# Performance work log

Hardware: AMD Instinct MI355X
Metric: run time of the kernel (lower is better)

The kernel has to match this reference:

```python
import jax, jax.numpy as jnp
import numpy as np

B, T, V, E, H, C = 128, 256, 50000, 300, 512, 11
START, STOP = 9, 10
NEG = -100000.0


def _lstm_dir(x, mask, w_ih, w_hh, b_ih, b_hh, reverse):
    # x: [B,T,D]; precompute input-to-gate projection for all timesteps
    gx = jnp.einsum('btd,gd->btg', x, w_ih) + b_ih + b_hh
    m = mask
    if reverse:
        gx = gx[:, ::-1]
        m = m[:, ::-1]
    Bc = x.shape[0]
    Hh = w_hh.shape[1]

    def step(carry, inp):
        h, c = carry
        g, mt = inp
        gates = g + h @ w_hh.T  # [B,4H]
        i, f, gg, o = jnp.split(gates, 4, axis=-1)
        i = jax.nn.sigmoid(i)
        f = jax.nn.sigmoid(f)
        o = jax.nn.sigmoid(o)
        gg = jnp.tanh(gg)
        c_new = f * c + i * gg
        h_new = o * jnp.tanh(c_new)
        mt = mt[:, None]
        h = jnp.where(mt, h_new, h)  # packed-sequence semantics: hold state on pads
        c = jnp.where(mt, c_new, c)
        return (h, c), h

    init = (jnp.zeros((Bc, Hh), x.dtype), jnp.zeros((Bc, Hh), x.dtype))
    _, hs = jax.lax.scan(step, init, (gx.transpose(1, 0, 2), m.T))
    hs = hs.transpose(1, 0, 2)
    if reverse:
        hs = hs[:, ::-1]
    # pad_packed_sequence zeroes padded positions
    return hs * mask[..., None].astype(x.dtype)


def _encode(tokens, mask, embeddings, params):
    x = embeddings[tokens]
    for (wif, whf, bif, bhf, wir, whr, bir, bhr) in params:
        fwd = _lstm_dir(x, mask, wif, whf, bif, bhf, False)
        bwd = _lstm_dir(x, mask, wir, whr, bir, bhr, True)
        x = jnp.concatenate([fwd, bwd], -1)
    return x


def _viterbi(emis, mask, transitions, seq_len):
    def vstep(scores, inp):
        emi, mt = inp
        cand = scores[:, :, None] + transitions[None]  # [B,C,C]
        bt = jnp.argmax(cand, axis=1)
        new = jnp.max(cand, axis=1) + emi
        return jnp.where(mt[:, None], new, scores), bt

    scores0 = jnp.zeros_like(emis[:, 0, :])
    final, backtrack = jax.lax.scan(vstep, scores0, (emis.transpose(1, 0, 2), mask.T))
    final = final + transitions[:, STOP][None]
    best_last = jnp.argmax(final, axis=-1)  # [B]

    ls = jnp.arange(emis.shape[1] - 1, -1, -1)

    def btstep(cur, inp):
        bt_l, l = inp
        emit = jnp.where(l < seq_len, cur, 0)  # pad tail with 0 as in original
        prev = jnp.take_along_axis(bt_l, cur[:, None], axis=1)[:, 0]
        cur = jnp.where((l >= 1) & (l <= seq_len - 1), prev, cur)
        return cur, emit

    _, emits = jax.lax.scan(btstep, best_last, (backtrack[::-1], ls))
    return emits[::-1].T  # [B,T]


def _nll(emis, tags, mask, transitions, seq_len):
    # CRF forward algorithm (replicates original init with -1e5 full scores)
    def fstep(scores, inp):
        emi, mt = inp
        new = jax.nn.logsumexp(scores[:, :, None] + emi[:, None, :] + transitions[None], axis=1)
        return jnp.where(mt[:, None], new, scores), None

    scores0 = jnp.full_like(emis[:, 0, :], NEG)
    final, _ = jax.lax.scan(fstep, scores0, (emis.transpose(1, 0, 2), mask.T))
    fwd_score = jax.nn.logsumexp(final + transitions[:, STOP][None], axis=-1, keepdims=True)

    em_sc = jnp.take_along_axis(emis, tags[..., None], -1)[..., 0]  # [B,T]
    y_aug = jnp.concatenate([jnp.full((tags.shape[0], 1), START, tags.dtype), tags], 1)
    tr_sc = transitions[y_aug[:, :-1], y_aug[:, 1:]]  # [B,T]
    last_tag = jnp.take_along_axis(y_aug, seq_len[:, None], 1)
    last_tr = transitions[last_tag[:, 0], STOP][:, None]
    mf = mask.astype(emis.dtype)
    gold = (mf * (em_sc + tr_sc)).sum(-1, keepdims=True) + last_tr
    return (fwd_score - gold).mean()


def setup_inputs() -> dict:
    key = jax.random.key(0)
    ks = iter(jax.random.split(key, 40))
    sl = jax.random.randint(next(ks), (B,), 1, T + 1)
    sl = -jnp.sort(-sl.at[0].set(T))  # descending, max == T (pack_padded requirement)
    mask = jnp.arange(T)[None, :] < sl[:, None]
    tokens = jax.random.randint(next(ks), (B, T), 0, V)
    tags = jax.random.randint(next(ks), (B, T), 0, 9)
    s = 1.0 / float(np.sqrt(H))

    def u(shape):
        return jax.random.uniform(next(ks), shape, jnp.float32, -s, s)

    inp = dict(tokens=tokens, seq_len=sl, mask=mask, tags=tags,
               embeddings=jax.random.normal(next(ks), (V, E), jnp.float32) * 0.1)
    G = 4 * H
    for li, d in enumerate([E, 2 * H]):
        for suf in ['', 'r']:
            inp[f'w_ih_l{li}{suf}'] = u((G, d))
            inp[f'w_hh_l{li}{suf}'] = u((G, H))
            inp[f'b_ih_l{li}{suf}'] = u((G,))
            inp[f'b_hh_l{li}{suf}'] = u((G,))
    inp['fc_w'] = u((C, 2 * H))
    inp['fc_b'] = u((C,))
    tr = jax.random.normal(next(ks), (C, C), jnp.float32)
    inp['transitions'] = tr.at[START, :].set(-1.0).at[:, STOP].set(-1.0)
    return inp


def reference(tokens, seq_len, mask, tags, embeddings,
              w_ih_l0, w_hh_l0, b_ih_l0, b_hh_l0,
              w_ih_l0r, w_hh_l0r, b_ih_l0r, b_hh_l0r,
              w_ih_l1, w_hh_l1, b_ih_l1, b_hh_l1,
              w_ih_l1r, w_hh_l1r, b_ih_l1r, b_hh_l1r,
              fc_w, fc_b, transitions):
    params = [(w_ih_l0, w_hh_l0, b_ih_l0, b_hh_l0, w_ih_l0r, w_hh_l0r, b_ih_l0r, b_hh_l0r),
              (w_ih_l1, w_hh_l1, b_ih_l1, b_hh_l1, w_ih_l1r, w_hh_l1r, b_ih_l1r, b_hh_l1r)]
    out = _encode(tokens, mask, embeddings, params)  # [B,T,2H]
    emis = jnp.einsum('bth,ch->btc', out, fc_w) + fc_b  # CRF fc (dropout=eval no-op)
    pred = _viterbi(emis, mask, transitions, seq_len)
    loss = _nll(emis, tags, mask, transitions, seq_len)
    return pred, loss
```

## Files before the change

### kernel.cpp

```cpp
#include <hip/hip_runtime.h>
#include <hip/hip_bf16.h>
#include <hip/hip_fp16.h>

#define BB   128
#define TT   256
#define EE   300
#define KP0  320
#define HH   512
#define GG   2048
#define NC   11
#define MM   (BB*TT)
#define START_TAG 9
#define STOP_TAG  10
#define NEGV (-100000.0f)

typedef _Float16 h2_t __attribute__((ext_vector_type(2)));
typedef _Float16 h4_t __attribute__((ext_vector_type(4)));
typedef _Float16 h8_t __attribute__((ext_vector_type(8)));
typedef float    f4_t __attribute__((ext_vector_type(4)));

__device__ __forceinline__ float sigf(float x) {
    return __builtin_amdgcn_rcpf(1.0f + __expf(-x));
}
__device__ __forceinline__ float tanh_fast(float x) {
    float e = __expf(2.0f * x);
    return 1.0f - 2.0f * __builtin_amdgcn_rcpf(e + 1.0f);
}

__device__ __forceinline__ void gload_lds16(const void* g, void* l) {
    __builtin_amdgcn_global_load_lds(
        (const __attribute__((address_space(1))) void*)(unsigned long long)(uintptr_t)g,
        (__attribute__((address_space(3))) void*)(unsigned int)(uintptr_t)l,
        16, 0, 0);
}

__global__ __launch_bounds__(256) void prep_kernel(float* out, int* flags,
                                                   const float* __restrict__ wi0,  _Float16* __restrict__ o0,
                                                   const float* __restrict__ wi0r, _Float16* __restrict__ o0r,
                                                   const float* __restrict__ wi1,  _Float16* __restrict__ o1,
                                                   const float* __restrict__ wi1r, _Float16* __restrict__ o1r) {
    const int b = blockIdx.x, tid = threadIdx.x;
    if (b == 0) {
        if (tid == 0) out[MM] = 0.0f;
        for (int i = tid; i < 1024; i += 256) flags[i] = 0;
    }
    const float* src; _Float16* dst; int K, Kp4, base;
    if (b < 640)       { src = wi0;  dst = o0;  K = EE;   Kp4 = 80;  base = 0; }
    else if (b < 1280) { src = wi0r; dst = o0r; K = EE;   Kp4 = 80;  base = 640; }
    else if (b < 3328) { src = wi1;  dst = o1;  K = 1024; Kp4 = 256; base = 1280; }
    else               { src = wi1r; dst = o1r; K = 1024; Kp4 = 256; base = 3328; }
    int idx = (b - base) * 256 + tid;
    int r = idx / Kp4, c4 = idx % Kp4, c = c4 * 4;
    h4_t v;
    if (c < K) {
        float4 f = *(const float4*)(src + (size_t)r * K + c);
        v[0] = (_Float16)f.x; v[1] = (_Float16)f.y; v[2] = (_Float16)f.z; v[3] = (_Float16)f.w;
    } else {
        v[0] = v[1] = v[2] = v[3] = (_Float16)0.0f;
    }
    *(h4_t*)(dst + (size_t)r * (Kp4 * 4) + c) = v;
}

__global__ __launch_bounds__(256) void embed16_kernel(const int* __restrict__ tok,
                                                      const float* __restrict__ emb,
                                                      _Float16* __restrict__ x0,
                                                      int total4) {
    int idx = blockIdx.x * 256 + threadIdx.x;
    if (idx >= total4) return;
    int m = idx / (KP0 / 4), c4 = idx % (KP0 / 4), c = c4 * 4;
    h4_t v;
    if (c < EE) {
        float4 f = *(const float4*)(emb + (size_t)tok[m] * EE + c);
        v[0] = (_Float16)f.x; v[1] = (_Float16)f.y; v[2] = (_Float16)f.z; v[3] = (_Float16)f.w;
    } else {
        v[0] = v[1] = v[2] = v[3] = (_Float16)0.0f;
    }
    *(h4_t*)(x0 + (size_t)m * KP0 + c) = v;
}

__global__ __launch_bounds__(256) void gemm_bt_kernel(const _Float16* __restrict__ A,
                                                      const _Float16* __restrict__ Wf,
                                                      const float* __restrict__ b1,
                                                      const float* __restrict__ b2,
                                                      _Float16* __restrict__ C,
                                                      int Kp) {
    __shared__ __align__(16) char smem[65536];
    _Float16* As0 = (_Float16*)smem;
    _Float16* Bs0 = (_Float16*)(smem + 16384);
    _Float16* As1 = (_Float16*)(smem + 32768);
    _Float16* Bs1 = (_Float16*)(smem + 49152);
    const int tid = threadIdx.x;
    const int m0 = blockIdx.y * 128, n0 = blockIdx.x * 128;
    const int wv = tid >> 6, lane = tid & 63;
    const int wm = wv & 1, wn = wv >> 1;
    const int col = lane & 15, quad = lane >> 4;
    const int rb = lane >> 3;
    const int cbs = ((lane & 7) * 8) ^ (rb << 3);
    const int rsw = (lane & 7) * 8;

    f4_t acc[4][4];
#pragma unroll
    for (int i = 0; i < 4; ++i)
#pragma unroll
        for (int j = 0; j < 4; ++j) acc[i][j] = (f4_t){0.f, 0.f, 0.f, 0.f};

#define STAGE(Ad, Bd, kk0)                                                              \
    _Pragma("unroll")                                                                   \
    for (int c = 0; c < 4; ++c) {                                                       \
        int slab = c * 32 + wv * 8;                                                     \
        gload_lds16(A  + (size_t)(m0 + slab + rb) * Kp + (kk0) + cbs, (Ad) + slab * 64);\
        gload_lds16(Wf + (size_t)(n0 + slab + rb) * Kp + (kk0) + cbs, (Bd) + slab * 64);\
    }

    const int nt = Kp >> 6;
    STAGE(As0, Bs0, 0);

    for (int t = 0; t < nt; ++t) {
        const _Float16* Ac = (t & 1) ? As1 : As0;
        const _Float16* Bc = (t & 1) ? Bs1 : Bs0;
        if (t + 1 < nt) {
            _Float16* An = (t & 1) ? As0 : As1;
            _Float16* Bn = (t & 1) ? Bs0 : Bs1;
            STAGE(An, Bn, (t + 1) * 64);
            asm volatile("s_waitcnt vmcnt(8)" ::: "memory");
        } else {
            asm volatile("s_waitcnt vmcnt(0)" ::: "memory");
        }
        __builtin_amdgcn_s_barrier();
        __builtin_amdgcn_sched_barrier(0);

#pragma unroll
        for (int kk = 0; kk < 2; ++kk) {
            h8_t af[4], bf[4];
#pragma unroll
            for (int i = 0; i < 4; ++i) {
                af[i] = *(const h8_t*)(Ac + (wm * 64 + i * 16 + col) * 64 + ((kk * 32 + quad * 8) ^ rsw));
                bf[i] = *(const h8_t*)(Bc + (wn * 64 + i * 16 + col) * 64 + ((kk * 32 + quad * 8) ^ rsw));
            }
#pragma unroll
            for (int mi = 0; mi < 4; ++mi)
#pragma unroll
                for (int ni = 0; ni < 4; ++ni)
                    acc[mi][ni] = __builtin_amdgcn_mfma_f32_16x16x32_f16(af[mi], bf[ni], acc[mi][ni], 0, 0, 0);
        }
        __builtin_amdgcn_sched_barrier(0);
        __builtin_amdgcn_s_barrier();
    }
#undef STAGE

    _Float16* Ct = (_Float16*)smem;
#pragma unroll
    for (int ni = 0; ni < 4; ++ni) {
        int n = n0 + wn * 64 + ni * 16 + col;
        float bias = b1[n] + b2[n];
#pragma unroll
        for (int mi = 0; mi < 4; ++mi) {
#pragma unroll
            for (int r = 0; r < 4; ++r) {
                int mrow = wm * 64 + mi * 16 + quad * 4 + r;
                Ct[mrow * 136 + wn * 64 + ni * 16 + col] = (_Float16)(acc[mi][ni][r] + bias);
            }
        }
    }
    __syncthreads();
    {
        int row = tid >> 1, half = tid & 1;
#pragma unroll
        for (int cc2 = 0; cc2 < 8; ++cc2) {
            h8_t v = *(const h8_t*)(Ct + row * 136 + half * 64 + cc2 * 8);
            *(h8_t*)(C + (size_t)(m0 + row) * GG + n0 + half * 64 + cc2 * 8) = v;
        }
    }
}

__global__ __launch_bounds__(256, 1) void lstm_rec3_kernel(
        const _Float16* __restrict__ gx_f, const _Float16* __restrict__ gx_r,
        const float* __restrict__ whh_f, const float* __restrict__ whh_r,
        const int* __restrict__ seqlen, int c0, int nbg,
        _Float16* __restrict__ hs, _Float16* __restrict__ hbuf, int* __restrict__ flags) {
    extern __shared__ _Float16 Wlds[];
    _Float16* hstage = Wlds + 32768;

    const int wg = blockIdx.x;
    const int gs = wg & 15;
    const int grp = wg >> 4;
    const int bg = grp % nbg;
    const int dir = grp / nbg;
    const _Float16* gx = dir ? gx_r : gx_f;
    const float* W = dir ? whh_r : whh_f;
    int* myFlags = flags + grp * 16;
    _Float16* hb = hbuf + (size_t)grp * 2 * 16384;

    const int tid = threadIdx.x;
    const int wv = tid >> 6, lane = tid & 63;
    const int mt = wv & 1;
    const int p  = wv >> 1;
    const int col = lane & 15, quad = lane >> 4;

    for (int e = tid; e < 4096; e += 256) {
        int ln = e & 63, kc = (e >> 6) & 15, nt = e >> 10;
        int pp = nt >> 1;
        int n_in_pair = ((nt & 1) << 4) + (ln & 15);
        int gt = n_in_pair >> 3, jj = n_in_pair & 7;
        int R = gt * 512 + gs * 16 + pp * 8 + jj;
        int k = kc * 32 + (ln >> 4) * 8;
        const float4* src = (const float4*)(W + (size_t)R * 512 + k);
        float4 f0 = src[0], f1 = src[1];
        h8_t v;
        v[0] = (_Float16)f0.x; v[1] = (_Float16)f0.y; v[2] = (_Float16)f0.z; v[3] = (_Float16)f0.w;
        v[4] = (_Float16)f1.x; v[5] = (_Float16)f1.y; v[6] = (_Float16)f1.z; v[7] = (_Float16)f1.w;
        *(h8_t*)(Wlds + (size_t)e * 8) = v;
    }
    __syncthreads();

    h8_t Bf0[16], Bf1[16];
#pragma unroll
    for (int kc = 0; kc < 16; ++kc) {
        Bf0[kc] = *(const h8_t*)(Wlds + (((p * 2 + 0) * 16 + kc) * 64 + lane) * 8);
        Bf1[kc] = *(const h8_t*)(Wlds + (((p * 2 + 1) * 16 + kc) * 64 + lane) * 8);
    }

    const int maxsl = seqlen[c0 + bg * 32];
    int sl_r[4];
#pragma unroll
    for (int r = 0; r < 4; ++r) sl_r[r] = seqlen[c0 + bg * 32 + mt * 16 + quad * 4 + r];

    const int jglob = gs * 16 + p * 8 + (col & 7);
    const int hi = col >> 3;

    _Float16 pg0[4], pg1[4];
#pragma unroll
    for (int r = 0; r < 4; ++r) {
        pg0[r] = (_Float16)0.0f; pg1[r] = (_Float16)0.0f;
        if (0 < sl_r[r]) {
            int tm = dir ? (sl_r[r] - 1) : 0;
            int b_loc = bg * 32 + mt * 16 + quad * 4 + r;
            size_t base = ((size_t)(b_loc * TT + tm)) * GG;
            pg0[r] = gx[base + hi * 512 + jglob];
            pg1[r] = gx[base + 1024 + hi * 512 + jglob];
        }
    }

    if (tid < 64) {
        int m = tid >> 1, half = tid & 1;
        h8_t z = {};
        const _Float16* dst = hb + 16384 + m * 512 + gs * 16 + half * 8;
        asm volatile("global_store_dwordx4 %0, %1, off sc0 sc1" :: "v"(dst), "v"(z) : "memory");
        asm volatile("s_waitcnt vmcnt(0)" ::: "memory");
        if (tid == 0) {
            int one = 1;
            asm volatile("global_store_dword %0, %1, off sc0 sc1" :: "v"(myFlags + gs), "v"(one) : "memory");
        }
    }

    float cst[4] = {0.f, 0.f, 0.f, 0.f};
    float hst[4] = {0.f, 0.f, 0.f, 0.f};

    for (int s = 0; s < maxsl; ++s) {
        if (tid < 16) {
            const int* fp = myFlags + tid;
            int v, it = 0;
            for (;;) {
                asm volatile("global_load_dword %0, %1, off sc0 sc1\n\ts_waitcnt vmcnt(0)"
                             : "=v"(v) : "v"(fp) : "memory");
                if (v >= s + 1) break;
                if (it < 3) __builtin_amdgcn_s_sleep(1);
                else        __builtin_amdgcn_s_sleep(4);
                ++it;
            }
        }
        __syncthreads();

        const _Float16* hrd = hb + ((s + 1) & 1) * 16384;
        _Float16* hwr = hb + (s & 1) * 16384;

        h8_t a[16];
        const _Float16* ap = hrd + (mt * 16 + col) * 512 + quad * 8;
#pragma unroll
        for (int kc = 0; kc < 16; ++kc)
            asm volatile("global_load_dwordx4 %0, %1, off sc0 sc1"
                         : "=v"(a[kc]) : "v"(ap + kc * 32));
        asm volatile("s_waitcnt vmcnt(0)" ::: "memory");
        __builtin_amdgcn_sched_barrier(0);

        f4_t acc0a = {0.f, 0.f, 0.f, 0.f}, acc0b = {0.f, 0.f, 0.f, 0.f};
        f4_t acc1a = {0.f, 0.f, 0.f, 0.f}, acc1b = {0.f, 0.f, 0.f, 0.f};
#pragma unroll
        for (int kc = 0; kc < 8; ++kc) {
            acc0a = __builtin_amdgcn_mfma_f32_16x16x32_f16(a[kc], Bf0[kc], acc0a, 0, 0, 0);
            acc1a = __builtin_amdgcn_mfma_f32_16x16x32_f16(a[kc], Bf1[kc], acc1a, 0, 0, 0);
        }
#pragma unroll
        for (int kc = 8; kc < 16; ++kc) {
            acc0b = __builtin_amdgcn_mfma_f32_16x16x32_f16(a[kc], Bf0[kc], acc0b, 0, 0, 0);
            acc1b = __builtin_amdgcn_mfma_f32_16x16x32_f16(a[kc], Bf1[kc], acc1b, 0, 0, 0);
        }
        f4_t acc0 = acc0a + acc0b;
        f4_t acc1 = acc1a + acc1b;

#pragma unroll
        for (int r = 0; r < 4; ++r) {
            const bool valid = (s < sl_r[r]);
            float a0 = acc0[r] + (float)pg0[r];
            float a1 = acc1[r] + (float)pg1[r];
            float x0v = __shfl_xor(a0, 8);
            float x1v = __shfl_xor(a1, 8);
            float gi = hi ? x0v : a0;
            float gf = hi ? a0 : x0v;
            float gg2 = hi ? x1v : a1;
            float go = hi ? a1 : x1v;
            if (valid) {
                float cn = sigf(gf) * cst[r] + sigf(gi) * tanh_fast(gg2);
                cst[r] = cn;
                hst[r] = sigf(go) * tanh_fast(cn);
            }
            if (!hi)
                hstage[(mt * 16 + quad * 4 + r) * 16 + p * 8 + (col & 7)] = (_Float16)hst[r];
        }
        __syncthreads();

        if (tid < 64) {
            int m = tid >> 1, half = tid & 1;
            h8_t v = *(const h8_t*)(hstage + m * 16 + half * 8);
            const _Float16* dst = hwr + m * 512 + gs * 16 + half * 8;
            asm volatile("global_store_dwordx4 %0, %1, off sc0 sc1" :: "v"(dst), "v"(v) : "memory");
            asm volatile("s_waitcnt vmcnt(0)" ::: "memory");
            if (tid == 0) {
                int fv = s + 2;
                asm volatile("global_store_dword %0, %1, off sc0 sc1" :: "v"(myFlags + gs), "v"(fv) : "memory");
            }
        }

#pragma unroll
        for (int r = 0; r < 4; ++r) {
            const bool valid = (s < sl_r[r]);
            if (valid && !hi) {
                int b_loc = bg * 32 + mt * 16 + quad * 4 + r;
                int tm = dir ? (sl_r[r] - 1 - s) : s;
                hs[((size_t)(b_loc * TT + tm) << 10) + (dir << 9) + jglob] = (_Float16)hst[r];
            }
        }
        {
            int sn = s + 1;
#pragma unroll
            for (int r = 0; r < 4; ++r) {
                pg0[r] = (_Float16)0.0f; pg1[r] = (_Float16)0.0f;
                if (sn < sl_r[r]) {
                    int tm = dir ? (sl_r[r] - 1 - sn) : sn;
                    int b_loc = bg * 32 + mt * 16 + quad * 4 + r;
                    size_t base = ((size_t)(b_loc * TT + tm)) * GG;
                    pg0[r] = gx[base + hi * 512 + jglob];
                    pg1[r] = gx[base + 1024 + hi * 512 + jglob];
                }
            }
        }
    }
}

__global__ __launch_bounds__(256) void emis_kernel(const _Float16* __restrict__ hs,
                                                   const float* __restrict__ fc_w,
                                                   const float* __restrict__ fc_b,
                                                   float* __restrict__ emis, int Mc) {
    __shared__ __align__(16) float Wl[NC * 1024];
    __shared__ float fb[NC];
    const int tid = threadIdx.x;
    {
        const float4* s4 = (const float4*)fc_w;
        float4* d4 = (float4*)Wl;
        for (int i = tid; i < NC * 256; i += 256) d4[i] = s4[i];
        if (tid < NC) fb[tid] = fc_b[tid];
    }
    __syncthreads();
    const int wv = tid >> 6, lane = tid & 63;

    for (int i = 0; i < 4; ++i) {
        int m = blockIdx.x * 16 + wv * 4 + i;
        if (m >= Mc) return;
        const h8_t* xp = (const h8_t*)(hs + (size_t)m * 1024);
        h8_t xa = xp[lane * 2], xb = xp[lane * 2 + 1];
        float xf[16];
#pragma unroll
        for (int j = 0; j < 8; ++j) { xf[j] = (float)xa[j]; xf[8 + j] = (float)xb[j]; }

        float s[NC];
#pragma unroll
        for (int c = 0; c < NC; ++c) {
            const float4* wr = (const float4*)(Wl + c * 1024 + lane * 16);
            float4 w0 = wr[0], w1 = wr[1], w2 = wr[2], w3 = wr[3];
            s[c] = xf[0] * w0.x + xf[1] * w0.y + xf[2] * w0.z + xf[3] * w0.w
                 + xf[4] * w1.x + xf[5] * w1.y + xf[6] * w1.z + xf[7] * w1.w
                 + xf[8] * w2.x + xf[9] * w2.y + xf[10] * w2.z + xf[11] * w2.w
                 + xf[12] * w3.x + xf[13] * w3.y + xf[14] * w3.z + xf[15] * w3.w;
        }
#pragma unroll
        for (int off = 32; off > 0; off >>= 1)
#pragma unroll
            for (int c = 0; c < NC; ++c) s[c] += __shfl_down(s[c], off);
        if (lane == 0) {
            float* eo = emis + (size_t)m * NC;
#pragma unroll
            for (int c = 0; c < NC; ++c) eo[c] = s[c] + fb[c];
        }
    }
}

__global__ __launch_bounds__(64) void crf_kernel(const float* __restrict__ emis,
                                                 const int* __restrict__ seq_len,
                                                 const int* __restrict__ tags,
                                                 const float* __restrict__ trans,
                                                 float* __restrict__ out, int c0) {
    const int b_loc = blockIdx.x;
    const int b = c0 + b_loc;
    const int lane = threadIdx.x;
    __shared__ float tr[NC * NC];
    __shared__ unsigned char btl[TT * NC];
    for (int i = lane; i < NC * NC; i += 64) tr[i] = trans[i];
    __syncthreads();
    const int sl = seq_len[b];
    const bool act = lane < NC;
    const int jj = act ? lane : 0;

    float vs = 0.0f;
    float ns = NEGV;

    float ej_cur = act ? emis[(size_t)(b_loc * TT) * NC + lane] : 0.0f;
    for (int t = 0; t < sl; ++t) {
        float ej_next = (act && t + 1 < sl) ? emis[(size_t)(b_loc * TT + t + 1) * NC + lane] : 0.0f;
        float vmax = -1e30f, nmax = -1e30f;
        int varg = 0;
        float nsave[NC];
#pragma unroll
        for (int i = 0; i < NC; ++i) {
            float vi = __shfl(vs, i);
            float ni = __shfl(ns, i);
            float tij = tr[i * NC + jj];
            float cv = vi + tij;
            if (cv > vmax) { vmax = cv; varg = i; }
            float cn = ni + tij;
            nsave[i] = cn;
            if (cn > nmax) nmax = cn;
        }
        float ssum = 0.f;
#pragma unroll
        for (int i = 0; i < NC; ++i) ssum += expf(nsave[i] - nmax);
        if (act) {
            vs = vmax + ej_cur;
            ns = nmax + logf(ssum) + ej_cur;
            btl[t * NC + lane] = (unsigned char)varg;
        }
        ej_cur = ej_next;
    }

    float finv = act ? vs + tr[lane * NC + STOP_TAG] : -1e30f;
    float finn = act ? ns + tr[lane * NC + STOP_TAG] : -1e30f;
    float vbest = -1e30f, fmax = -1e30f;
    int barg = 0;
#pragma unroll
    for (int j = 0; j < NC; ++j) {
        float v = __shfl(finv, j);
        if (v > vbest) { vbest = v; barg = j; }
        float n = __shfl(finn, j);
        if (n > fmax) fmax = n;
    }
    float fsum = 0.f;
#pragma unroll
    for (int j = 0; j < NC; ++j) fsum += expf(__shfl(finn, j) - fmax);
    float fwd = fmax + logf(fsum);

    float gsum = 0.f;
    for (int t = lane; t < sl; t += 64) {
        int tg = tags[b * TT + t];
        int pv = (t == 0) ? START_TAG : tags[b * TT + t - 1];
        gsum += emis[(size_t)(b_loc * TT + t) * NC + tg] + tr[pv * NC + tg];
    }
#pragma unroll
    for (int off = 32; off > 0; off >>= 1) gsum += __shfl_down(gsum, off);

    if (lane == 0) {
        float gold = gsum + tr[tags[b * TT + sl - 1] * NC + STOP_TAG];
        atomicAdd(out + MM, (fwd - gold) * (1.0f / (float)BB));
        int cur = barg;
        for (int l = sl - 1; l >= 0; --l) {
            out[b * TT + l] = (float)cur;
            if (l >= 1) cur = (int)btl[l * NC + cur];
        }
    }
    for (int l = sl + lane; l < TT; l += 64) out[b * TT + l] = 0.0f;
}

extern "C" void kernel_launch(void* const* d_in, const int* in_sizes, int n_in,
                              void* d_out, int out_size, void* d_ws, size_t ws_size,
                              hipStream_t stream) {
    (void)in_sizes; (void)n_in; (void)out_size;
    const int* tokens = (const int*)d_in[0];
    const int* seqlen = (const int*)d_in[1];
    const int* tags = (const int*)d_in[3];
    const float* emb = (const float*)d_in[4];
    const float* w_ih_l0  = (const float*)d_in[5];
    const float* w_hh_l0  = (const float*)d_in[6];
    const float* b_ih_l0  = (const float*)d_in[7];
    const float* b_hh_l0  = (const float*)d_in[8];
    const float* w_ih_l0r = (const float*)d_in[9];
    const float* w_hh_l0r = (const float*)d_in[10];
    const float* b_ih_l0r = (const float*)d_in[11];
    const float* b_hh_l0r = (const float*)d_in[12];
    const float* w_ih_l1  = (const float*)d_in[13];
    const float* w_hh_l1  = (const float*)d_in[14];
    const float* b_ih_l1  = (const float*)d_in[15];
    const float* b_hh_l1  = (const float*)d_in[16];
    const float* w_ih_l1r = (const float*)d_in[17];
    const float* w_hh_l1r = (const float*)d_in[18];
    const float* b_ih_l1r = (const float*)d_in[19];
    const float* b_hh_l1r = (const float*)d_in[20];
    const float* fc_w  = (const float*)d_in[21];
    const float* fc_b  = (const float*)d_in[22];
    const float* trans = (const float*)d_in[23];

    const size_t per_b = 2097152u + 524288u + 163840u + 11264u + 2816u;
    const size_t fixed = 524288u + 4096u + 2u * 1310720u + 2u * 4194304u;
    int Bc = 128;
    while (Bc > 32 && fixed + per_b * (size_t)Bc > ws_size) Bc >>= 1;

    char* ws = (char*)d_ws;
    _Float16* hbuf = (_Float16*)ws;
    int* flags = (int*)(ws + 524288u);
    _Float16* w0f = (_Float16*)(ws + 528384u);
    _Float16* w0r = (_Float16*)(ws + 528384u + 1310720u);
    _Float16* w1f = (_Float16*)(ws + 528384u + 2u * 1310720u);
    _Float16* w1r = (_Float16*)(ws + 528384u + 2u * 1310720u + 4194304u);
    char* p = ws + fixed;
    _Float16* gxf   = (_Float16*)p;   p += (size_t)Bc * 1048576u;
    _Float16* gxr   = (_Float16*)p;   p += (size_t)Bc * 1048576u;
    _Float16* hs    = (_Float16*)p;   p += (size_t)Bc * 524288u;
    _Float16* x0f16 = (_Float16*)p;   p += (size_t)Bc * 163840u;
    float* emis     = (float*)p;      p += (size_t)Bc * 11264u;
    float* out = (float*)d_out;

    prep_kernel<<<5376, 256, 0, stream>>>(out, flags,
                                          w_ih_l0, w0f, w_ih_l0r, w0r,
                                          w_ih_l1, w1f, w_ih_l1r, w1r);

    const int nbg = Bc / 32;
    const int nchunk = BB / Bc;
    for (int cidx = 0; cidx < nchunk; ++cidx) {
        const int c0 = cidx * Bc;
        const int Mc = Bc * TT;
        dim3 gdim(GG / 128, Mc / 128);
        int* fl_l0 = flags + (cidx * 2 + 0) * 128;
        int* fl_l1 = flags + (cidx * 2 + 1) * 128;

        embed16_kernel<<<(Mc * 80 + 255) / 256, 256, 0, stream>>>(tokens + c0 * TT, emb, x0f16, Mc * 80);
        gemm_bt_kernel<<<gdim, 256, 0, stream>>>(x0f16, w0f, b_ih_l0,  b_hh_l0,  gxf, KP0);
        gemm_bt_kernel<<<gdim, 256, 0, stream>>>(x0f16, w0r, b_ih_l0r, b_hh_l0r, gxr, KP0);
        lstm_rec3_kernel<<<2 * nbg * 16, 256, 66560, stream>>>(
            gxf, gxr, w_hh_l0, w_hh_l0r, seqlen, c0, nbg, hs, hbuf, fl_l0);
        gemm_bt_kernel<<<gdim, 256, 0, stream>>>(hs, w1f, b_ih_l1,  b_hh_l1,  gxf, 1024);
        gemm_bt_kernel<<<gdim, 256, 0, stream>>>(hs, w1r, b_ih_l1r, b_hh_l1r, gxr, 1024);
        lstm_rec3_kernel<<<2 * nbg * 16, 256, 66560, stream>>>(
            gxf, gxr, w_hh_l1, w_hh_l1r, seqlen, c0, nbg, hs, hbuf, fl_l1);
        emis_kernel<<<Mc / 16, 256, 0, stream>>>(hs, fc_w, fc_b, emis, Mc);
        crf_kernel<<<Bc, 64, 0, stream>>>(emis, seqlen, tags, trans, out, c0);
    }
}
```

Measured before the change: 4.828 ms.

## Detect same-XCD recurrence groups and relax coherence bits; merge fwd/rev input GEMMs

Result: slower. 4.934 ms (+2.2%).

```diff
diff --git a/kernel.cpp b/kernel.cpp
--- a/kernel.cpp
+++ b/kernel.cpp
@@ -41,7 +41,11 @@
                                                    const float* __restrict__ wi1r, _Float16* __restrict__ o1r) {
     const int b = blockIdx.x, tid = threadIdx.x;
     if (b == 0) {
-        if (tid == 0) out[MM] = 0.0f;
+        if (tid == 0) {
+            out[MM] = 0.0f;
+            unsigned eb = (unsigned)__builtin_amdgcn_s_memrealtime();
+            flags[1153] = (int)(eb | 1u);
+        }
         for (int i = tid; i < 1024; i += 256) flags[i] = 0;
     }
     const float* src; _Float16* dst; int K, Kp4, base;
@@ -78,19 +82,28 @@
     *(h4_t*)(x0 + (size_t)m * KP0 + c) = v;
 }
 
-__global__ __launch_bounds__(256) void gemm_bt_kernel(const _Float16* __restrict__ A,
-                                                      const _Float16* __restrict__ Wf,
-                                                      const float* __restrict__ b1,
-                                                      const float* __restrict__ b2,
-                                                      _Float16* __restrict__ C,
-                                                      int Kp) {
+__global__ __launch_bounds__(256) void gemm_bt2_kernel(const _Float16* __restrict__ A,
+                                                       const _Float16* __restrict__ Wfp,
+                                                       const _Float16* __restrict__ Wrp,
+                                                       const float* __restrict__ b1f,
+                                                       const float* __restrict__ b2f,
+                                                       const float* __restrict__ b1r,
+                                                       const float* __restrict__ b2r,
+                                                       _Float16* __restrict__ Cf,
+                                                       _Float16* __restrict__ Cr,
+                                                       int Kp) {
     __shared__ __align__(16) char smem[65536];
     _Float16* As0 = (_Float16*)smem;
     _Float16* Bs0 = (_Float16*)(smem + 16384);
     _Float16* As1 = (_Float16*)(smem + 32768);
     _Float16* Bs1 = (_Float16*)(smem + 49152);
     const int tid = threadIdx.x;
-    const int m0 = blockIdx.y * 128, n0 = blockIdx.x * 128;
+    const int dir = blockIdx.x >> 4;
+    const _Float16* Wf = dir ? Wrp : Wfp;
+    _Float16* C = dir ? Cr : Cf;
+    const float* b1 = dir ? b1r : b1f;
+    const float* b2 = dir ? b2r : b2f;
+    const int m0 = blockIdx.y * 128, n0 = (blockIdx.x & 15) * 128;
     const int wv = tid >> 6, lane = tid & 63;
     const int wm = wv & 1, wn = wv >> 1;
     const int col = lane & 15, quad = lane >> 4;
@@ -177,18 +190,21 @@
         const _Float16* __restrict__ gx_f, const _Float16* __restrict__ gx_r,
         const float* __restrict__ whh_f, const float* __restrict__ whh_r,
         const int* __restrict__ seqlen, int c0, int nbg,
-        _Float16* __restrict__ hs, _Float16* __restrict__ hbuf, int* __restrict__ flags) {
+        _Float16* __restrict__ hs, _Float16* __restrict__ hbuf,
+        int* __restrict__ flagsB, int foff, int dd) {
     extern __shared__ _Float16 Wlds[];
     _Float16* hstage = Wlds + 32768;
 
     const int wg = blockIdx.x;
-    const int gs = wg & 15;
-    const int grp = wg >> 4;
+    int gs, grp;
+    if (2 * nbg == 8) { grp = wg & 7; gs = wg >> 3; }
+    else              { gs = wg & 15; grp = wg >> 4; }
     const int bg = grp % nbg;
     const int dir = grp / nbg;
     const _Float16* gx = dir ? gx_r : gx_f;
     const float* W = dir ? whh_r : whh_f;
-    int* myFlags = flags + grp * 16;
+    int* myFlags = flagsB + foff + grp * 16;
+    int* det = flagsB + 1024 + grp * 16;
     _Float16* hb = hbuf + (size_t)grp * 2 * 16384;
 
     const int tid = threadIdx.x;
@@ -220,6 +236,36 @@
         Bf1[kc] = *(const h8_t*)(Wlds + (((p * 2 + 1) * 16 + kc) * 64 + lane) * 8);
     }
 
+    int xcc;
+    asm volatile("s_getreg_b32 %0, hwreg(HW_REG_XCC_ID)" : "=s"(xcc));
+    xcc &= 63;
+    const unsigned ebase = (unsigned)flagsB[1153];
+    const int ep = (int)((ebase + (unsigned)dd) << 6);
+    if (tid == 0) {
+        int mv = ep | xcc;
+        asm volatile("global_store_dword %0, %1, off sc0 sc1" :: "v"(det + gs), "v"(mv) : "memory");
+    }
+    asm volatile("s_waitcnt vmcnt(0)" ::: "memory");
+    if (wv == 0) {
+        int v = ep | xcc;
+        if (lane < 16) {
+            const int* fp = det + lane;
+            int it = 0;
+            for (;;) {
+                asm volatile("global_load_dword %0, %1, off sc0 sc1\n\ts_waitcnt vmcnt(0)"
+                             : "=v"(v) : "v"(fp) : "memory");
+                if ((v & ~63) == ep) break;
+                if (it >= 4) __builtin_amdgcn_s_sleep(2);
+                ++it;
+            }
+        }
+        unsigned long long bal = __ballot((v & 63) == xcc);
+        if (lane == 0) *(volatile int*)hstage = (bal == ~0ull) ? 1 : 0;
+    }
+    __syncthreads();
+    const int fast = *(volatile int*)hstage;
+    __syncthreads();
+
     const int maxsl = seqlen[c0 + bg * 32];
     int sl_r[4];
 #pragma unroll
@@ -245,11 +291,13 @@
         int m = tid >> 1, half = tid & 1;
         h8_t z = {};
         const _Float16* dst = hb + 16384 + m * 512 + gs * 16 + half * 8;
-        asm volatile("global_store_dwordx4 %0, %1, off sc0 sc1" :: "v"(dst), "v"(z) : "memory");
+        if (fast) asm volatile("global_store_dwordx4 %0, %1, off sc0"     :: "v"(dst), "v"(z) : "memory");
+        else      asm volatile("global_store_dwordx4 %0, %1, off sc0 sc1" :: "v"(dst), "v"(z) : "memory");
         asm volatile("s_waitcnt vmcnt(0)" ::: "memory");
         if (tid == 0) {
             int one = 1;
-            asm volatile("global_store_dword %0, %1, off sc0 sc1" :: "v"(myFlags + gs), "v"(one) : "memory");
+            if (fast) asm volatile("global_store_dword %0, %1, off sc0"     :: "v"(myFlags + gs), "v"(one) : "memory");
+            else      asm volatile("global_store_dword %0, %1, off sc0 sc1" :: "v"(myFlags + gs), "v"(one) : "memory");
         }
     }
 
@@ -260,13 +308,23 @@
         if (tid < 16) {
             const int* fp = myFlags + tid;
             int v, it = 0;
-            for (;;) {
-                asm volatile("global_load_dword %0, %1, off sc0 sc1\n\ts_waitcnt vmcnt(0)"
-                             : "=v"(v) : "v"(fp) : "memory");
-                if (v >= s + 1) break;
-                if (it < 3) __builtin_amdgcn_s_sleep(1);
-                else        __builtin_amdgcn_s_sleep(4);
-                ++it;
+            if (fast) {
+                for (;;) {
+                    asm volatile("global_load_dword %0, %1, off sc0\n\ts_waitcnt vmcnt(0)"
+                                 : "=v"(v) : "v"(fp) : "memory");
+                    if (v >= s + 1) break;
+                    if (it >= 32) __builtin_amdgcn_s_sleep(1);
+                    ++it;
+                }
+            } else {
+                for (;;) {
+                    asm volatile("global_load_dword %0, %1, off sc0 sc1\n\ts_waitcnt vmcnt(0)"
+                                 : "=v"(v) : "v"(fp) : "memory");
+                    if (v >= s + 1) break;
+                    if (it < 3) __builtin_amdgcn_s_sleep(1);
+                    else        __builtin_amdgcn_s_sleep(4);
+                    ++it;
+                }
             }
         }
         __syncthreads();
@@ -276,10 +334,17 @@
 
         h8_t a[16];
         const _Float16* ap = hrd + (mt * 16 + col) * 512 + quad * 8;
-#pragma unroll
-        for (int kc = 0; kc < 16; ++kc)
-            asm volatile("global_load_dwordx4 %0, %1, off sc0 sc1"
-                         : "=v"(a[kc]) : "v"(ap + kc * 32));
+        if (fast) {
+#pragma unroll
+            for (int kc = 0; kc < 16; ++kc)
+                asm volatile("global_load_dwordx4 %0, %1, off sc0"
+                             : "=v"(a[kc]) : "v"(ap + kc * 32));
+        } else {
+#pragma unroll
+            for (int kc = 0; kc < 16; ++kc)
+                asm volatile("global_load_dwordx4 %0, %1, off sc0 sc1"
+                             : "=v"(a[kc]) : "v"(ap + kc * 32));
+        }
         asm volatile("s_waitcnt vmcnt(0)" ::: "memory");
         __builtin_amdgcn_sched_barrier(0);
 
@@ -323,11 +388,13 @@
             int m = tid >> 1, half = tid & 1;
             h8_t v = *(const h8_t*)(hstage + m * 16 + half * 8);
             const _Float16* dst = hwr + m * 512 + gs * 16 + half * 8;
-            asm volatile("global_store_dwordx4 %0, %1, off sc0 sc1" :: "v"(dst), "v"(v) : "memory");
+            if (fast) asm volatile("global_store_dwordx4 %0, %1, off sc0"     :: "v"(dst), "v"(v) : "memory");
+            else      asm volatile("global_store_dwordx4 %0, %1, off sc0 sc1" :: "v"(dst), "v"(v) : "memory");
             asm volatile("s_waitcnt vmcnt(0)" ::: "memory");
             if (tid == 0) {
                 int fv = s + 2;
-                asm volatile("global_store_dword %0, %1, off sc0 sc1" :: "v"(myFlags + gs), "v"(fv) : "memory");
+                if (fast) asm volatile("global_store_dword %0, %1, off sc0"     :: "v"(myFlags + gs), "v"(fv) : "memory");
+                else      asm volatile("global_store_dword %0, %1, off sc0 sc1" :: "v"(myFlags + gs), "v"(fv) : "memory");
             }
         }
 
@@ -517,17 +584,17 @@
     const float* trans = (const float*)d_in[23];
 
     const size_t per_b = 2097152u + 524288u + 163840u + 11264u + 2816u;
-    const size_t fixed = 524288u + 4096u + 2u * 1310720u + 2u * 4194304u;
+    const size_t fixed = 524288u + 8192u + 2u * 1310720u + 2u * 4194304u;
     int Bc = 128;
     while (Bc > 32 && fixed + per_b * (size_t)Bc > ws_size) Bc >>= 1;
 
     char* ws = (char*)d_ws;
     _Float16* hbuf = (_Float16*)ws;
     int* flags = (int*)(ws + 524288u);
-    _Float16* w0f = (_Float16*)(ws + 528384u);
-    _Float16* w0r = (_Float16*)(ws + 528384u + 1310720u);
-    _Float16* w1f = (_Float16*)(ws + 528384u + 2u * 1310720u);
-    _Float16* w1r = (_Float16*)(ws + 528384u + 2u * 1310720u + 4194304u);
+    _Float16* w0f = (_Float16*)(ws + 532480u);
+    _Float16* w0r = (_Float16*)(ws + 532480u + 1310720u);
+    _Float16* w1f = (_Float16*)(ws + 532480u + 2u * 1310720u);
+    _Float16* w1r = (_Float16*)(ws + 532480u + 2u * 1310720u + 4194304u);
     char* p = ws + fixed;
     _Float16* gxf   = (_Float16*)p;   p += (size_t)Bc * 1048576u;
     _Float16* gxr   = (_Float16*)p;   p += (size_t)Bc * 1048576u;
@@ -545,19 +612,21 @@
     for (int cidx = 0; cidx < nchunk; ++cidx) {
         const int c0 = cidx * Bc;
         const int Mc = Bc * TT;
-        dim3 gdim(GG / 128, Mc / 128);
-        int* fl_l0 = flags + (cidx * 2 + 0) * 128;
-        int* fl_l1 = flags + (cidx * 2 + 1) * 128;
+        dim3 g2(32, Mc / 128);
 
         embed16_kernel<<<(Mc * 80 + 255) / 256, 256, 0, stream>>>(tokens + c0 * TT, emb, x0f16, Mc * 80);
-        gemm_bt_kernel<<<gdim, 256, 0, stream>>>(x0f16, w0f, b_ih_l0,  b_hh_l0,  gxf, KP0);
-        gemm_bt_kernel<<<gdim, 256, 0, stream>>>(x0f16, w0r, b_ih_l0r, b_hh_l0r, gxr, KP0);
+        gemm_bt2_kernel<<<g2, 256, 0, stream>>>(x0f16, w0f, w0r,
+                                                b_ih_l0, b_hh_l0, b_ih_l0r, b_hh_l0r,
+                                                gxf, gxr, KP0);
         lstm_rec3_kernel<<<2 * nbg * 16, 256, 66560, stream>>>(
-            gxf, gxr, w_hh_l0, w_hh_l0r, seqlen, c0, nbg, hs, hbuf, fl_l0);
-        gemm_bt_kernel<<<gdim, 256, 0, stream>>>(hs, w1f, b_ih_l1,  b_hh_l1,  gxf, 1024);
-        gemm_bt_kernel<<<gdim, 256, 0, stream>>>(hs, w1r, b_ih_l1r, b_hh_l1r, gxr, 1024);
+            gxf, gxr, w_hh_l0, w_hh_l0r, seqlen, c0, nbg, hs, hbuf,
+            flags, (cidx * 2 + 0) * 128, cidx * 2 + 0);
+        gemm_bt2_kernel<<<g2, 256, 0, stream>>>(hs, w1f, w1r,
+                                                b_ih_l1, b_hh_l1, b_ih_l1r, b_hh_l1r,
+                                                gxf, gxr, 1024);
         lstm_rec3_kernel<<<2 * nbg * 16, 256, 66560, stream>>>(
-            gxf, gxr, w_hh_l1, w_hh_l1r, seqlen, c0, nbg, hs, hbuf, fl_l1);
+            gxf, gxr, w_hh_l1, w_hh_l1r, seqlen, c0, nbg, hs, hbuf,
+            flags, (cidx * 2 + 1) * 128, cidx * 2 + 1);
         emis_kernel<<<Mc / 16, 256, 0, stream>>>(hs, fc_w, fc_b, emis, Mc);
         crf_kernel<<<Bc, 64, 0, stream>>>(emis, seqlen, tags, trans, out, c0);
     }
```
